# Kernel tuning notes

Hardware: AMD Instinct MI355X
Metric: run time of the kernel (lower is better)

Reference implementation:

```python
import jax, jax.numpy as jnp
import numpy as np

D_MODEL = 1024
N_HEADS = 16
HEAD_DIM = D_MODEL // N_HEADS
B, S = 4, 2048


def setup_inputs() -> dict:
    key = jax.random.key(0)
    ks = jax.random.split(key, 12)
    s = 1.0 / np.sqrt(D_MODEL)
    inp = {
        'query': jax.random.normal(ks[0], (B, S, D_MODEL), jnp.float32),
        'key': jax.random.normal(ks[1], (B, S, D_MODEL), jnp.float32),
        'value': jax.random.normal(ks[2], (B, S, D_MODEL), jnp.float32),
        # causal mask, broadcast over batch and heads: [1,1,S,S]
        'mask': jnp.tril(jnp.ones((S, S), jnp.int32))[None, None],
        'Wq': jax.random.normal(ks[3], (D_MODEL, D_MODEL), jnp.float32) * s,
        'bq': jnp.zeros((D_MODEL,), jnp.float32),
        'Wk': jax.random.normal(ks[4], (D_MODEL, D_MODEL), jnp.float32) * s,
        'bk': jnp.zeros((D_MODEL,), jnp.float32),
        'Wv': jax.random.normal(ks[5], (D_MODEL, D_MODEL), jnp.float32) * s,
        'bv': jnp.zeros((D_MODEL,), jnp.float32),
        'Wo': jax.random.normal(ks[6], (D_MODEL, D_MODEL), jnp.float32) * s,
        'bo': jnp.zeros((D_MODEL,), jnp.float32),
    }
    return inp


def reference(query, key, value, mask, Wq, bq, Wk, bk, Wv, bv, Wo, bo):
    b, q_len, _ = query.shape
    scale = jnp.sqrt(jnp.float32(HEAD_DIM))
    # projections
    q = query @ Wq + bq
    k = key @ Wk + bk
    v = value @ Wv + bv
    # [b, h, s, hd]
    q = q.reshape(b, q_len, N_HEADS, HEAD_DIM).transpose(0, 2, 1, 3)
    k = k.reshape(b, -1, N_HEADS, HEAD_DIM).transpose(0, 2, 1, 3)
    v = v.reshape(b, -1, N_HEADS, HEAD_DIM).transpose(0, 2, 1, 3)
    scores = jnp.einsum('bhqd,bhkd->bhqk', q, k) / scale
    scores = jnp.where(mask == 0, jnp.float32(-jnp.inf), scores)
    attn = jax.nn.softmax(scores, axis=-1)  # dropout p=0 / eval mode
    out = jnp.einsum('bhqk,bhkd->bhqd', attn, v)
    out = out.transpose(0, 2, 1, 3).reshape(b, q_len, D_MODEL)
    return out @ Wo + bo
```

## Files before the change

kernel.cpp:

```cpp
#include <hip/hip_runtime.h>
#include <hip/hip_bf16.h>

typedef __attribute__((ext_vector_type(8))) short short8;
typedef __attribute__((ext_vector_type(4))) float floatx4;
typedef __attribute__((ext_vector_type(4))) unsigned short ushort4v;

#define D_MODEL 1024
#define S_LEN   2048
#define N_HEADS 16
#define HEAD_DIM 64
#define BATCH   4

__device__ __forceinline__ unsigned short f2bf(float x) {
    union { float f; unsigned int u; } v; v.f = x;
    unsigned int u = v.u;
    unsigned int r = (u + 0x7FFFu + ((u >> 16) & 1u)) >> 16;
    return (unsigned short)r;
}
__device__ __forceinline__ unsigned short f2bf_trunc(float x) {
    union { float f; unsigned int u; } v; v.f = x;
    return (unsigned short)(v.u >> 16);
}

__device__ __forceinline__ void gload_lds16(const void* g, void* s) {
    __builtin_amdgcn_global_load_lds(
        (const __attribute__((address_space(1))) void*)g,
        (__attribute__((address_space(3))) void*)s, 16, 0, 0);
}

struct Conv3 {
    const float* src[3];
    unsigned short* dst[3];
};

__global__ __launch_bounds__(256) void conv_bf16(Conv3 a) {
    const float* s = a.src[blockIdx.z];
    unsigned short* d = a.dst[blockIdx.z];
    size_t i = ((size_t)blockIdx.x * 256 + threadIdx.x) * 8;
    float4 f0 = *(const float4*)(s + i);
    float4 f1 = *(const float4*)(s + i + 4);
    short8 v;
    v[0] = (short)f2bf(f0.x); v[1] = (short)f2bf(f0.y);
    v[2] = (short)f2bf(f0.z); v[3] = (short)f2bf(f0.w);
    v[4] = (short)f2bf(f1.x); v[5] = (short)f2bf(f1.y);
    v[6] = (short)f2bf(f1.z); v[7] = (short)f2bf(f1.w);
    *(short8*)(d + i) = v;
}

struct Trans4 {
    const float* W[4];
    unsigned short* Wt[4];
};

__global__ __launch_bounds__(256) void transpose_w(Trans4 args) {
    __shared__ unsigned short tile[32][33];
    const float* W = args.W[blockIdx.z];
    unsigned short* Wt = args.Wt[blockIdx.z];
    int n0 = blockIdx.x * 32;
    int k0 = blockIdx.y * 32;
    int t = threadIdx.x;
    int r = t >> 5, c = t & 31;
    for (int i = 0; i < 4; ++i) {
        int k = k0 + r + i * 8;
        tile[r + i * 8][c] = f2bf(W[(size_t)k * D_MODEL + n0 + c]);
    }
    __syncthreads();
    for (int i = 0; i < 4; ++i) {
        int n = n0 + r + i * 8;
        Wt[(size_t)n * D_MODEL + k0 + c] = tile[c][r + i * 8];
    }
}

struct GemmIn {
    const unsigned short* A;
    const unsigned short* Bt;
    const float* bias;
    void* C;
    int mode;
};
struct Gemm3 { GemmIn g[3]; };

#define BAR()   asm volatile("s_barrier" ::: "memory")
#define LGKM0() asm volatile("s_waitcnt lgkmcnt(0)" ::: "memory")
#define VMW2()  asm volatile("s_waitcnt vmcnt(2)" ::: "memory")
#define VMW0()  asm volatile("s_waitcnt vmcnt(0)" ::: "memory")

#define READ_A(BUF, I0)                                                        \
    _Pragma("unroll") for (int ii = 0; ii < 4; ++ii) {                         \
        aF[ii][0] = *(const short8*)&lds[(BUF)*24576 + aOff + ((I0)+ii)*512];  \
        aF[ii][1] = *(const short8*)&lds[(BUF)*24576 + aOff + ((I0)+ii)*512 + 4096]; \
    }
#define READ_B(BUF)                                                            \
    _Pragma("unroll") for (int jj = 0; jj < 2; ++jj) {                         \
        bF[jj][0] = *(const short8*)&lds[(BUF)*24576 + bOff + jj*512];         \
        bF[jj][1] = *(const short8*)&lds[(BUF)*24576 + bOff + jj*512 + 4096];  \
    }
#define MFMA_Q(I0)                                                             \
    __builtin_amdgcn_s_setprio(1);                                             \
    _Pragma("unroll") for (int ii = 0; ii < 4; ++ii)                           \
    _Pragma("unroll") for (int jj = 0; jj < 2; ++jj) {                         \
        acc[(I0)+ii][jj] = __builtin_amdgcn_mfma_f32_16x16x32_bf16(            \
            aF[ii][0], bF[jj][0], acc[(I0)+ii][jj], 0, 0, 0);                  \
        acc[(I0)+ii][jj] = __builtin_amdgcn_mfma_f32_16x16x32_bf16(            \
            aF[ii][1], bF[jj][1], acc[(I0)+ii][jj], 0, 0, 0);                  \
    }                                                                          \
    __builtin_amdgcn_s_setprio(0)

__global__ __launch_bounds__(512, 2) void gemm_256(Gemm3 args) {
    constexpr int K = D_MODEL, N = D_MODEL;
    constexpr int NT = K / 64;
    constexpr int NI = NT / 2;
    GemmIn g = args.g[blockIdx.z];

    __shared__ __align__(16) unsigned short lds[49152];

    const int m0 = blockIdx.x * 256;
    const int n0 = blockIdx.y * 128;
    const int t = threadIdx.x;
    const int w = t >> 6, lane = t & 63;
    const int quad = lane >> 4, l16 = lane & 15;
    const int wm = w >> 2, wn = w & 3;

    const int srow = w * 16 + (lane >> 2);
    const int scol = ((lane & 3) * 8) ^ ((lane & 32) ? 16 : 0);

    const int fx = (quad * 8) ^ ((l16 & 8) ? 16 : 0);
    const int aOff = wm * 8192 + l16 * 32 + fx;
    const int bOff = 16384 + (wn * 32 + l16) * 32 + fx;

    floatx4 acc[8][2] = {};
    short8 aF[4][2], bF[2][2];

    auto stageA = [&](int buf, int h, int kt) {
        const unsigned short* src =
            g.A + (size_t)(m0 + h * 128 + srow) * K + kt * 64 + scol;
        unsigned short* dst = &lds[buf * 24576 + h * 8192 + w * 512];
        gload_lds16(src, dst);
        gload_lds16(src + 32, dst + 4096);
    };
    auto stageB = [&](int buf, int kt) {
        const unsigned short* src =
            g.Bt + (size_t)(n0 + srow) * K + kt * 64 + scol;
        unsigned short* dst = &lds[buf * 24576 + 16384 + w * 512];
        gload_lds16(src, dst);
        gload_lds16(src + 32, dst + 4096);
    };

    stageA(0, 0, 0); stageA(0, 1, 0); stageB(0, 0);
    stageB(1, 1);
    VMW2();
    BAR();

    for (int n = 0; n < NI - 1; ++n) {
        const int t0 = 2 * n;
        READ_A(0, 0); READ_B(0);
        stageA(1, 0, t0 + 1); stageA(1, 1, t0 + 1);
        BAR(); LGKM0();
        MFMA_Q(0);
        BAR();
        READ_A(0, 4);
        stageB(0, t0 + 2);
        VMW2();
        BAR(); LGKM0();
        MFMA_Q(4);
        BAR();
        READ_A(1, 0); READ_B(1);
        stageA(0, 0, t0 + 2); stageA(0, 1, t0 + 2);
        BAR(); LGKM0();
        MFMA_Q(0);
        BAR();
        READ_A(1, 4);
        stageB(1, t0 + 3);
        VMW2();
        BAR(); LGKM0();
        MFMA_Q(4);
        BAR();
    }

    {
        READ_A(0, 0); READ_B(0);
        stageA(1, 0, NT - 1); stageA(1, 1, NT - 1);
        BAR(); LGKM0();
        MFMA_Q(0);
        BAR();
        READ_A(0, 4);
        VMW0();
        BAR(); LGKM0();
        MFMA_Q(4);
        BAR();
        READ_A(1, 0); READ_B(1);
        BAR(); LGKM0();
        MFMA_Q(0);
        BAR();
        READ_A(1, 4);
        LGKM0();
        MFMA_Q(4);
    }

    if (g.mode == 2) {
        unsigned short* Ct = (unsigned short*)g.C;
#pragma unroll
        for (int j = 0; j < 2; ++j) {
            int col = n0 + wn * 32 + j * 16 + l16;
            int h = col >> 6, dd = col & 63;
            float bv = g.bias[col];
#pragma unroll
            for (int i = 0; i < 8; ++i) {
                int row0 = m0 + wm * 128 + i * 16 + quad * 4;
                int bb = row0 >> 11, s = row0 & 2047;
                ushort4v u;
#pragma unroll
                for (int r = 0; r < 4; ++r) u[r] = f2bf(acc[i][j][r] + bv);
                *(ushort4v*)(Ct + ((size_t)(bb * 16 + h) * 64 + dd) * 2048 + s) = u;
            }
        }
    } else {
#pragma unroll
        for (int j = 0; j < 2; ++j) {
            int col = n0 + wn * 32 + j * 16 + l16;
            float bv = g.bias[col];
#pragma unroll
            for (int i = 0; i < 8; ++i) {
#pragma unroll
                for (int r = 0; r < 4; ++r) {
                    int row = m0 + wm * 128 + i * 16 + quad * 4 + r;
                    float v = acc[i][j][r] + bv;
                    if (g.mode == 1)
                        ((float*)g.C)[(size_t)row * N + col] = v;
                    else
                        ((unsigned short*)g.C)[(size_t)row * N + col] = f2bf(v);
                }
            }
        }
    }
}

__global__ __launch_bounds__(512) void flash_attn(
    const unsigned short* __restrict__ Qp,
    const unsigned short* __restrict__ Kp,
    const unsigned short* __restrict__ Vtg,
    unsigned short* __restrict__ Op) {
    constexpr int S = S_LEN, D = D_MODEL;
    __shared__ __align__(16) unsigned short Ks[64 * 64];
    __shared__ __align__(16) unsigned short Vs[64 * 64];
    __shared__ __align__(16) unsigned short Ps[8][16][72];

    int pair = blockIdx.x;
    int bh = blockIdx.y;
    int b = bh >> 4;
    int t = threadIdx.x;
    int wave = t >> 6, lane = t & 63;
    int quad = lane >> 4, l16 = lane & 15;

    const size_t head_off = (size_t)b * S * D + (size_t)(bh & 15) * HEAD_DIM;
    const unsigned short* Khead = Kp + head_off;
    const unsigned short* Vhead = Vtg + (size_t)bh * 64 * S;

    int q0l = pair * 128, q0h = (15 - pair) * 128;
    int qgl = q0l + wave * 16 + l16;
    int qgh = q0h + wave * 16 + l16;

    const unsigned short* qpl = Qp + head_off + (size_t)qgl * D + quad * 8;
    short8 ql0 = *(const short8*)qpl, ql1 = *(const short8*)(qpl + 32);
    const unsigned short* qph = Qp + head_off + (size_t)qgh * D + quad * 8;
    short8 qh0 = *(const short8*)qph, qh1 = *(const short8*)(qph + 32);

    floatx4 ol[4] = {}, oh[4] = {};
    float ll = 0.f, lh = 0.f;
    const float cs = 0.125f * 1.44269504088896340736f;

    int sw = wave & 3;
    bool doK = wave < 4;
    int srow = sw * 16 + (lane >> 2);
    int scol = (lane & 3) * 8;
    unsigned short* sdst0 = (doK ? Ks : Vs) + sw * 512;
    unsigned short* sdst1 = sdst0 + 2048;

    int wqminl = q0l + wave * 16, wqmaxl = wqminl + 15;
    int wqminh = q0h + wave * 16, wqmaxh = wqminh + 15;

    auto half_step = [&](int k0, int qg, int wqmin, float& l_i,
                         floatx4* o, short8 qb0, short8 qb1) {
        floatx4 st[4];
        for (int gk = 0; gk < 4; ++gk) {
            short8 ka0 = *(const short8*)&Ks[(gk * 16 + l16) * 32 + quad * 8];
            short8 ka1 = *(const short8*)&Ks[2048 + (gk * 16 + l16) * 32 + quad * 8];
            floatx4 s = {};
            s = __builtin_amdgcn_mfma_f32_16x16x32_bf16(ka0, qb0, s, 0, 0, 0);
            s = __builtin_amdgcn_mfma_f32_16x16x32_bf16(ka1, qb1, s, 0, 0, 0);
            st[gk] = s;
        }

        float sv[16];
        float rs = 0.f;
        if (k0 + 63 < wqmin) {
            for (int i = 0; i < 16; ++i) {
                sv[i] = __builtin_amdgcn_exp2f(st[i >> 2][i & 3] * cs);
                rs += sv[i];
            }
        } else {
            for (int gk = 0; gk < 4; ++gk)
                for (int r = 0; r < 4; ++r) {
                    int key = k0 + gk * 16 + quad * 4 + r;
                    float p = (key <= qg)
                        ? __builtin_amdgcn_exp2f(st[gk][r] * cs) : 0.f;
                    sv[gk * 4 + r] = p;
                    rs += p;
                }
        }
        rs += __shfl_xor(rs, 16);
        rs += __shfl_xor(rs, 32);
        l_i += rs;

        for (int gk = 0; gk < 4; ++gk) {
            ushort4v u;
            for (int r = 0; r < 4; ++r) u[r] = f2bf_trunc(sv[gk * 4 + r]);
            *(ushort4v*)&Ps[wave][l16][gk * 16 + quad * 4] = u;
        }

        short8 pf0 = *(const short8*)&Ps[wave][l16][quad * 8];
        short8 pf1 = *(const short8*)&Ps[wave][l16][32 + quad * 8];
        for (int jd = 0; jd < 4; ++jd) {
            short8 va0 = *(const short8*)&Vs[(jd * 16 + l16) * 32 + quad * 8];
            short8 va1 = *(const short8*)&Vs[2048 + (jd * 16 + l16) * 32 + quad * 8];
            o[jd] = __builtin_amdgcn_mfma_f32_16x16x32_bf16(va0, pf0, o[jd], 0, 0, 0);
            o[jd] = __builtin_amdgcn_mfma_f32_16x16x32_bf16(va1, pf1, o[jd], 0, 0, 0);
        }
    };

    int n_kt = 2 * (15 - pair) + 2;
    for (int kt = 0; kt < n_kt; ++kt) {
        int k0 = kt * 64;
        if (doK) {
            gload_lds16(Khead + (size_t)(k0 + srow) * D + scol, sdst0);
            gload_lds16(Khead + (size_t)(k0 + srow) * D + 32 + scol, sdst1);
        } else {
            gload_lds16(Vhead + (size_t)srow * S + k0 + scol, sdst0);
            gload_lds16(Vhead + (size_t)srow * S + k0 + 32 + scol, sdst1);
        }
        __syncthreads();

        if (k0 <= wqmaxl) half_step(k0, qgl, wqminl, ll, ol, ql0, ql1);
        if (k0 <= wqmaxh) half_step(k0, qgh, wqminh, lh, oh, qh0, qh1);
        __syncthreads();
    }

    {
        float inv = 1.0f / ll;
        unsigned short* op = Op + head_off + (size_t)qgl * D;
        for (int jd = 0; jd < 4; ++jd) {
            ushort4v u;
            for (int r = 0; r < 4; ++r) u[r] = f2bf(ol[jd][r] * inv);
            *(ushort4v*)(op + jd * 16 + quad * 4) = u;
        }
    }
    {
        float inv = 1.0f / lh;
        unsigned short* op = Op + head_off + (size_t)qgh * D;
        for (int jd = 0; jd < 4; ++jd) {
            ushort4v u;
            for (int r = 0; r < 4; ++r) u[r] = f2bf(oh[jd][r] * inv);
            *(ushort4v*)(op + jd * 16 + quad * 4) = u;
        }
    }
}

extern "C" void kernel_launch(void* const* d_in, const int* in_sizes, int n_in,
                              void* d_out, int out_size, void* d_ws,
                              size_t ws_size, hipStream_t stream) {
    const float* query = (const float*)d_in[0];
    const float* key   = (const float*)d_in[1];
    const float* value = (const float*)d_in[2];
    const float* Wq = (const float*)d_in[4];
    const float* bq = (const float*)d_in[5];
    const float* Wk = (const float*)d_in[6];
    const float* bk = (const float*)d_in[7];
    const float* Wv = (const float*)d_in[8];
    const float* bv = (const float*)d_in[9];
    const float* Wo = (const float*)d_in[10];
    const float* bo = (const float*)d_in[11];
    float* out = (float*)d_out;

    char* ws = (char*)d_ws;
    const size_t WT_SZ = (size_t)D_MODEL * D_MODEL * 2;
    const size_t X_SZ = (size_t)BATCH * S_LEN * D_MODEL * 2;
    unsigned short* wtq = (unsigned short*)(ws);
    unsigned short* wtk = (unsigned short*)(ws + WT_SZ);
    unsigned short* wtv = (unsigned short*)(ws + 2 * WT_SZ);
    unsigned short* wto = (unsigned short*)(ws + 3 * WT_SZ);
    unsigned short* Qbf = (unsigned short*)(ws + 4 * WT_SZ);
    unsigned short* Kbf = (unsigned short*)(ws + 4 * WT_SZ + X_SZ);
    unsigned short* Vbf = (unsigned short*)(ws + 4 * WT_SZ + 2 * X_SZ);
    unsigned short* Qp  = (unsigned short*)(ws + 4 * WT_SZ + 3 * X_SZ);
    unsigned short* Kp  = (unsigned short*)(ws + 4 * WT_SZ + 4 * X_SZ);
    unsigned short* Vtg = (unsigned short*)(ws + 4 * WT_SZ + 5 * X_SZ);
    unsigned short* Ao  = Qbf;

    Trans4 ta;
    ta.W[0] = Wq; ta.W[1] = Wk; ta.W[2] = Wv; ta.W[3] = Wo;
    ta.Wt[0] = wtq; ta.Wt[1] = wtk; ta.Wt[2] = wtv; ta.Wt[3] = wto;
    transpose_w<<<dim3(32, 32, 4), 256, 0, stream>>>(ta);

    Conv3 ca;
    ca.src[0] = query; ca.src[1] = key; ca.src[2] = value;
    ca.dst[0] = Qbf;   ca.dst[1] = Kbf; ca.dst[2] = Vbf;
    conv_bf16<<<dim3(4096, 1, 3), 256, 0, stream>>>(ca);

    Gemm3 gq;
    gq.g[0].A = Qbf; gq.g[0].Bt = wtq; gq.g[0].bias = bq; gq.g[0].C = Qp;  gq.g[0].mode = 0;
    gq.g[1].A = Kbf; gq.g[1].Bt = wtk; gq.g[1].bias = bk; gq.g[1].C = Kp;  gq.g[1].mode = 0;
    gq.g[2].A = Vbf; gq.g[2].Bt = wtv; gq.g[2].bias = bv; gq.g[2].C = Vtg; gq.g[2].mode = 2;
    gemm_256<<<dim3(32, 8, 3), 512, 0, stream>>>(gq);

    flash_attn<<<dim3(8, BATCH * N_HEADS), 512, 0, stream>>>(
        Qp, Kp, Vtg, Ao);

    Gemm3 go;
    go.g[0].A = Ao; go.g[0].Bt = wto; go.g[0].bias = bo; go.g[0].C = out; go.g[0].mode = 1;
    gemm_256<<<dim3(32, 8, 1), 512, 0, stream>>>(go);
}
```

Measured before the change: 336.3 us.

## Shrink projection GEMM to 128x128 tiles with 4 waves and new staging

Replaces the 256x128, 8-wave GEMM with a 128x128 tile using 4 waves. Each wave computes a 64x64 sub-tile and B fragments alternate between two register sets, and the launch grid doubles. This yields more blocks (1536 for QKV, 512 for the output projection) across the 256 CUs and smaller LDS use, improving wave fill and occupancy. The price is less operand reuse per block and a more serialized pipeline, since each half-step now waits with vmcnt(0).

```diff
diff --git a/kernel.cpp b/kernel.cpp
--- a/kernel.cpp
+++ b/kernel.cpp
@@ -82,131 +82,132 @@
 
 #define BAR()   asm volatile("s_barrier" ::: "memory")
 #define LGKM0() asm volatile("s_waitcnt lgkmcnt(0)" ::: "memory")
-#define VMW2()  asm volatile("s_waitcnt vmcnt(2)" ::: "memory")
 #define VMW0()  asm volatile("s_waitcnt vmcnt(0)" ::: "memory")
 
-#define READ_A(BUF, I0)                                                        \
+#define READ_A4(BUF)                                                           \
     _Pragma("unroll") for (int ii = 0; ii < 4; ++ii) {                         \
-        aF[ii][0] = *(const short8*)&lds[(BUF)*24576 + aOff + ((I0)+ii)*512];  \
-        aF[ii][1] = *(const short8*)&lds[(BUF)*24576 + aOff + ((I0)+ii)*512 + 4096]; \
-    }
-#define READ_B(BUF)                                                            \
+        aF[ii][0] = *(const short8*)&lds[(BUF)*16384 + aOff + ii*512];         \
+        aF[ii][1] = *(const short8*)&lds[(BUF)*16384 + aOff + ii*512 + 4096];  \
+    }
+#define READ_B2(BUF, J0, DST)                                                  \
     _Pragma("unroll") for (int jj = 0; jj < 2; ++jj) {                         \
-        bF[jj][0] = *(const short8*)&lds[(BUF)*24576 + bOff + jj*512];         \
-        bF[jj][1] = *(const short8*)&lds[(BUF)*24576 + bOff + jj*512 + 4096];  \
-    }
-#define MFMA_Q(I0)                                                             \
+        DST[jj][0] = *(const short8*)&lds[(BUF)*16384 + bOff + ((J0)+jj)*512]; \
+        DST[jj][1] = *(const short8*)&lds[(BUF)*16384 + bOff + ((J0)+jj)*512 + 4096]; \
+    }
+#define MFMA_H(J0, BREG)                                                       \
     __builtin_amdgcn_s_setprio(1);                                             \
     _Pragma("unroll") for (int ii = 0; ii < 4; ++ii)                           \
     _Pragma("unroll") for (int jj = 0; jj < 2; ++jj) {                         \
-        acc[(I0)+ii][jj] = __builtin_amdgcn_mfma_f32_16x16x32_bf16(            \
-            aF[ii][0], bF[jj][0], acc[(I0)+ii][jj], 0, 0, 0);                  \
-        acc[(I0)+ii][jj] = __builtin_amdgcn_mfma_f32_16x16x32_bf16(            \
-            aF[ii][1], bF[jj][1], acc[(I0)+ii][jj], 0, 0, 0);                  \
+        acc[ii][(J0)+jj] = __builtin_amdgcn_mfma_f32_16x16x32_bf16(            \
+            aF[ii][0], BREG[jj][0], acc[ii][(J0)+jj], 0, 0, 0);                \
+        acc[ii][(J0)+jj] = __builtin_amdgcn_mfma_f32_16x16x32_bf16(            \
+            aF[ii][1], BREG[jj][1], acc[ii][(J0)+jj], 0, 0, 0);                \
     }                                                                          \
     __builtin_amdgcn_s_setprio(0)
 
-__global__ __launch_bounds__(512, 2) void gemm_256(Gemm3 args) {
+__global__ __launch_bounds__(256, 2) void gemm_128(Gemm3 args) {
     constexpr int K = D_MODEL, N = D_MODEL;
     constexpr int NT = K / 64;
     constexpr int NI = NT / 2;
     GemmIn g = args.g[blockIdx.z];
 
-    __shared__ __align__(16) unsigned short lds[49152];
-
-    const int m0 = blockIdx.x * 256;
+    __shared__ __align__(16) unsigned short lds[32768];
+
+    const int m0 = blockIdx.x * 128;
     const int n0 = blockIdx.y * 128;
     const int t = threadIdx.x;
     const int w = t >> 6, lane = t & 63;
     const int quad = lane >> 4, l16 = lane & 15;
-    const int wm = w >> 2, wn = w & 3;
-
-    const int srow = w * 16 + (lane >> 2);
+    const int wm = w >> 1, wn = w & 1;
+
+    const int srow = w * 32 + (lane >> 2);
     const int scol = ((lane & 3) * 8) ^ ((lane & 32) ? 16 : 0);
 
     const int fx = (quad * 8) ^ ((l16 & 8) ? 16 : 0);
-    const int aOff = wm * 8192 + l16 * 32 + fx;
-    const int bOff = 16384 + (wn * 32 + l16) * 32 + fx;
-
-    floatx4 acc[8][2] = {};
-    short8 aF[4][2], bF[2][2];
-
-    auto stageA = [&](int buf, int h, int kt) {
-        const unsigned short* src =
-            g.A + (size_t)(m0 + h * 128 + srow) * K + kt * 64 + scol;
-        unsigned short* dst = &lds[buf * 24576 + h * 8192 + w * 512];
-        gload_lds16(src, dst);
-        gload_lds16(src + 32, dst + 4096);
+    const int aOff = (wm * 64 + l16) * 32 + fx;
+    const int bOff = 8192 + (wn * 64 + l16) * 32 + fx;
+
+    floatx4 acc[4][4] = {};
+    short8 aF[4][2], bE[2][2], bO[2][2];
+
+    auto stageA = [&](int buf, int kt) {
+        const unsigned short* s0 = g.A + (size_t)(m0 + srow) * K + kt * 64 + scol;
+        unsigned short* d0 = &lds[buf * 16384 + (w * 32) * 32];
+        gload_lds16(s0, d0);
+        gload_lds16(s0 + 32, d0 + 4096);
+        gload_lds16(s0 + (size_t)16 * K, d0 + 512);
+        gload_lds16(s0 + (size_t)16 * K + 32, d0 + 512 + 4096);
     };
     auto stageB = [&](int buf, int kt) {
-        const unsigned short* src =
-            g.Bt + (size_t)(n0 + srow) * K + kt * 64 + scol;
-        unsigned short* dst = &lds[buf * 24576 + 16384 + w * 512];
-        gload_lds16(src, dst);
-        gload_lds16(src + 32, dst + 4096);
+        const unsigned short* s0 = g.Bt + (size_t)(n0 + srow) * K + kt * 64 + scol;
+        unsigned short* d0 = &lds[buf * 16384 + 8192 + (w * 32) * 32];
+        gload_lds16(s0, d0);
+        gload_lds16(s0 + 32, d0 + 4096);
+        gload_lds16(s0 + (size_t)16 * K, d0 + 512);
+        gload_lds16(s0 + (size_t)16 * K + 32, d0 + 512 + 4096);
     };
 
-    stageA(0, 0, 0); stageA(0, 1, 0); stageB(0, 0);
-    stageB(1, 1);
-    VMW2();
+    stageA(0, 0); stageB(0, 0);
+    VMW0();
     BAR();
 
     for (int n = 0; n < NI - 1; ++n) {
         const int t0 = 2 * n;
-        READ_A(0, 0); READ_B(0);
-        stageA(1, 0, t0 + 1); stageA(1, 1, t0 + 1);
-        BAR(); LGKM0();
-        MFMA_Q(0);
-        BAR();
-        READ_A(0, 4);
+        READ_A4(0); READ_B2(0, 0, bE);
+        stageB(1, t0 + 1);
+        BAR(); LGKM0();
+        MFMA_H(0, bE);
+        BAR();
+        READ_B2(0, 2, bO);
+        stageA(1, t0 + 1);
+        BAR(); LGKM0();
+        MFMA_H(2, bO);
+        VMW0();
+        BAR();
+        READ_A4(1); READ_B2(1, 0, bE);
         stageB(0, t0 + 2);
-        VMW2();
-        BAR(); LGKM0();
-        MFMA_Q(4);
-        BAR();
-        READ_A(1, 0); READ_B(1);
-        stageA(0, 0, t0 + 2); stageA(0, 1, t0 + 2);
-        BAR(); LGKM0();
-        MFMA_Q(0);
-        BAR();
-        READ_A(1, 4);
-        stageB(1, t0 + 3);
-        VMW2();
-        BAR(); LGKM0();
-        MFMA_Q(4);
+        BAR(); LGKM0();
+        MFMA_H(0, bE);
+        BAR();
+        READ_B2(1, 2, bO);
+        stageA(0, t0 + 2);
+        BAR(); LGKM0();
+        MFMA_H(2, bO);
+        VMW0();
         BAR();
     }
 
     {
-        READ_A(0, 0); READ_B(0);
-        stageA(1, 0, NT - 1); stageA(1, 1, NT - 1);
-        BAR(); LGKM0();
-        MFMA_Q(0);
-        BAR();
-        READ_A(0, 4);
+        READ_A4(0); READ_B2(0, 0, bE);
+        stageB(1, NT - 1);
+        BAR(); LGKM0();
+        MFMA_H(0, bE);
+        BAR();
+        READ_B2(0, 2, bO);
+        stageA(1, NT - 1);
+        BAR(); LGKM0();
+        MFMA_H(2, bO);
         VMW0();
-        BAR(); LGKM0();
-        MFMA_Q(4);
-        BAR();
-        READ_A(1, 0); READ_B(1);
-        BAR(); LGKM0();
-        MFMA_Q(0);
-        BAR();
-        READ_A(1, 4);
+        BAR();
+        READ_A4(1); READ_B2(1, 0, bE);
+        BAR(); LGKM0();
+        MFMA_H(0, bE);
+        BAR();
+        READ_B2(1, 2, bO);
         LGKM0();
-        MFMA_Q(4);
+        MFMA_H(2, bO);
     }
 
     if (g.mode == 2) {
         unsigned short* Ct = (unsigned short*)g.C;
 #pragma unroll
-        for (int j = 0; j < 2; ++j) {
-            int col = n0 + wn * 32 + j * 16 + l16;
+        for (int j = 0; j < 4; ++j) {
+            int col = n0 + wn * 64 + j * 16 + l16;
             int h = col >> 6, dd = col & 63;
             float bv = g.bias[col];
 #pragma unroll
-            for (int i = 0; i < 8; ++i) {
-                int row0 = m0 + wm * 128 + i * 16 + quad * 4;
+            for (int i = 0; i < 4; ++i) {
+                int row0 = m0 + wm * 64 + i * 16 + quad * 4;
                 int bb = row0 >> 11, s = row0 & 2047;
                 ushort4v u;
 #pragma unroll
@@ -216,14 +217,14 @@
         }
     } else {
 #pragma unroll
-        for (int j = 0; j < 2; ++j) {
-            int col = n0 + wn * 32 + j * 16 + l16;
+        for (int j = 0; j < 4; ++j) {
+            int col = n0 + wn * 64 + j * 16 + l16;
             float bv = g.bias[col];
 #pragma unroll
-            for (int i = 0; i < 8; ++i) {
+            for (int i = 0; i < 4; ++i) {
 #pragma unroll
                 for (int r = 0; r < 4; ++r) {
-                    int row = m0 + wm * 128 + i * 16 + quad * 4 + r;
+                    int row = m0 + wm * 64 + i * 16 + quad * 4 + r;
                     float v = acc[i][j][r] + bv;
                     if (g.mode == 1)
                         ((float*)g.C)[(size_t)row * N + col] = v;
@@ -410,12 +411,12 @@
     gq.g[0].A = Qbf; gq.g[0].Bt = wtq; gq.g[0].bias = bq; gq.g[0].C = Qp;  gq.g[0].mode = 0;
     gq.g[1].A = Kbf; gq.g[1].Bt = wtk; gq.g[1].bias = bk; gq.g[1].C = Kp;  gq.g[1].mode = 0;
     gq.g[2].A = Vbf; gq.g[2].Bt = wtv; gq.g[2].bias = bv; gq.g[2].C = Vtg; gq.g[2].mode = 2;
-    gemm_256<<<dim3(32, 8, 3), 512, 0, stream>>>(gq);
+    gemm_128<<<dim3(64, 8, 3), 256, 0, stream>>>(gq);
 
     flash_attn<<<dim3(8, BATCH * N_HEADS), 512, 0, stream>>>(
         Qp, Kp, Vtg, Ao);
 
     Gemm3 go;
     go.g[0].A = Ao; go.g[0].Bt = wto; go.g[0].bias = bo; go.g[0].C = out; go.g[0].mode = 1;
-    gemm_256<<<dim3(32, 8, 1), 512, 0, stream>>>(go);
-}
+    gemm_128<<<dim3(64, 8, 1), 256, 0, stream>>>(go);
+}
```

Result: no change. 329.8 us (-2.0%).
